# Kernel optimization log

Hardware: AMD Instinct MI355X
Metric: run time of the kernel (lower is better)

Reference implementation:

```python
import jax, jax.numpy as jnp
import numpy as np
from jax import lax

T, B, C, H, W = 8, 32, 256, 32, 32
EPS = 1e-12


def setup_inputs() -> dict:
    key = jax.random.key(0)
    k1, k2, k3, k4 = jax.random.split(key, 4)
    return {
        "x_accum": jax.random.normal(k1, (T, B, C, H, W), dtype=jnp.float32),
        "prev_scale": jax.random.uniform(k2, (C,), dtype=jnp.float32, minval=0.1, maxval=1.0),
        "prev_bias": jax.random.normal(k3, (C,), dtype=jnp.float32),
        "vth": jax.random.uniform(k4, (C,), dtype=jnp.float32, minval=0.5, maxval=1.5),
        "tau": jnp.ones((1,), dtype=jnp.float32) * 4.0,
        "is_first_layer": 0,
    }


def reference(x_accum, prev_scale, prev_bias, vth, tau, is_first_layer):
    # per-channel views broadcasting over [B, C, H, W]
    s = prev_scale.reshape(1, C, 1, 1)
    b = prev_bias.reshape(1, C, 1, 1)
    v = vth.reshape(1, C, 1, 1)
    tau = tau.reshape(())  # scalar
    bias_scaled = jnp.round(b * tau / (s + EPS))
    vth_scaled = jnp.round(v * tau / (s + EPS))

    drive = x_accum if is_first_layer else x_accum * tau  # [T, B, C, H, W]

    def step(mem, x_t):
        mem = mem + x_t + bias_scaled
        spike = (mem >= vth_scaled).astype(x_accum.dtype)
        mem = mem - spike * vth_scaled  # soft reset
        return mem, spike

    mem0 = jnp.zeros_like(x_accum[0])
    _, spikes = lax.scan(step, mem0, drive)
    return spikes  # [T, B, C, H, W]
```

## Files before the change

kernel.cpp:

```cpp
#include <hip/hip_runtime.h>


#define T_STEPS 8
#define C_CH    256
#define HW      1024
#define EPS_F   1e-12f

typedef float v4f __attribute__((ext_vector_type(4)));

__global__ __launch_bounds__(256) void integer_neuron_kernel(
    const float* __restrict__ x,
    const float* __restrict__ prev_scale,
    const float* __restrict__ prev_bias,
    const float* __restrict__ vth,
    const float* __restrict__ tau_p,
    const int*   __restrict__ is_first_p,
    float* __restrict__ out,
    long long n_planes)
{
    const float tau      = tau_p[0];
    const int   is_first = is_first_p[0];
    const float drive_mul = is_first ? 1.0f : tau;

    const long long plane = (long long)blockIdx.x;
    const int c = (int)(plane % C_CH);

    const float denom       = __fadd_rn(prev_scale[c], EPS_F);
    const float bias_scaled = rintf(__fdiv_rn(__fmul_rn(prev_bias[c], tau), denom));
    const float vth_scaled  = rintf(__fdiv_rn(__fmul_rn(vth[c],       tau), denom));

    const long long N    = n_planes * (long long)HW;
    const long long base = plane * (long long)HW + (long long)threadIdx.x * 4;

    float mx = 0.0f, my = 0.0f, mz = 0.0f, mw = 0.0f;

    #pragma unroll
    for (int t = 0; t < T_STEPS; ++t) {
        const long long off = (long long)t * N + base;
        const v4f xv = __builtin_nontemporal_load(
            reinterpret_cast<const v4f*>(x + off));

        v4f sp;

        mx    = __fadd_rn(__fadd_rn(mx, __fmul_rn(xv.x, drive_mul)), bias_scaled);
        sp.x  = (mx >= vth_scaled) ? 1.0f : 0.0f;
        mx    = __fsub_rn(mx, __fmul_rn(sp.x, vth_scaled));
        my    = __fadd_rn(__fadd_rn(my, __fmul_rn(xv.y, drive_mul)), bias_scaled);
        sp.y  = (my >= vth_scaled) ? 1.0f : 0.0f;
        my    = __fsub_rn(my, __fmul_rn(sp.y, vth_scaled));
        mz    = __fadd_rn(__fadd_rn(mz, __fmul_rn(xv.z, drive_mul)), bias_scaled);
        sp.z  = (mz >= vth_scaled) ? 1.0f : 0.0f;
        mz    = __fsub_rn(mz, __fmul_rn(sp.z, vth_scaled));
        mw    = __fadd_rn(__fadd_rn(mw, __fmul_rn(xv.w, drive_mul)), bias_scaled);
        sp.w  = (mw >= vth_scaled) ? 1.0f : 0.0f;
        mw    = __fsub_rn(mw, __fmul_rn(sp.w, vth_scaled));

        __builtin_nontemporal_store(sp, reinterpret_cast<v4f*>(out + off));
    }
}

extern "C" void kernel_launch(void* const* d_in, const int* in_sizes, int n_in,
                              void* d_out, int out_size, void* d_ws, size_t ws_size,
                              hipStream_t stream) {
    const float* x          = (const float*)d_in[0];
    const float* prev_scale = (const float*)d_in[1];
    const float* prev_bias  = (const float*)d_in[2];
    const float* vth        = (const float*)d_in[3];
    const float* tau        = (const float*)d_in[4];
    const int*   is_first   = (const int*)d_in[5];
    float* out = (float*)d_out;

    const long long total    = (long long)out_size;
    const long long n_planes = total / ((long long)T_STEPS * HW);

    dim3 grid((unsigned)n_planes);
    dim3 block(256);
    integer_neuron_kernel<<<grid, block, 0, stream>>>(
        x, prev_scale, prev_bias, vth, tau, is_first, out, n_planes);
}
```

Before: 100.1 us.

## Map one wavefront per plane with four vec4 loads per thread per step

Each 256-thread block now covers four channel planes, one 64-lane wavefront per plane. Each thread handles four float4 positions strided by 256 floats, so it issues four independent 16-byte loads per timestep. The grid shrinks by four. The aim is more memory-level parallelism per thread and fewer blocks for this bandwidth-bound kernel, at the cost of more registers and fewer resident waves.

```diff
diff --git a/kernel.cpp b/kernel.cpp
--- a/kernel.cpp
+++ b/kernel.cpp
@@ -5,6 +5,7 @@
 #define C_CH    256
 #define HW      1024
 #define EPS_F   1e-12f
+#define NPOS    4
 
 typedef float v4f __attribute__((ext_vector_type(4)));
 
@@ -22,7 +23,7 @@
     const int   is_first = is_first_p[0];
     const float drive_mul = is_first ? 1.0f : tau;
 
-    const long long plane = (long long)blockIdx.x;
+    const long long plane = (long long)blockIdx.x * 4 + (threadIdx.x >> 6);
     const int c = (int)(plane % C_CH);
 
     const float denom       = __fadd_rn(prev_scale[c], EPS_F);
@@ -30,32 +31,43 @@
     const float vth_scaled  = rintf(__fdiv_rn(__fmul_rn(vth[c],       tau), denom));
 
     const long long N    = n_planes * (long long)HW;
-    const long long base = plane * (long long)HW + (long long)threadIdx.x * 4;
+    const long long base = plane * (long long)HW
+                         + (long long)(threadIdx.x & 63) * 4;
 
-    float mx = 0.0f, my = 0.0f, mz = 0.0f, mw = 0.0f;
+    float mem[NPOS][4];
+    #pragma unroll
+    for (int p = 0; p < NPOS; ++p)
+        #pragma unroll
+        for (int j = 0; j < 4; ++j)
+            mem[p][j] = 0.0f;
 
     #pragma unroll
     for (int t = 0; t < T_STEPS; ++t) {
         const long long off = (long long)t * N + base;
-        const v4f xv = __builtin_nontemporal_load(
-            reinterpret_cast<const v4f*>(x + off));
 
-        v4f sp;
+        v4f xv[NPOS];
+        #pragma unroll
+        for (int p = 0; p < NPOS; ++p)
+            xv[p] = __builtin_nontemporal_load(
+                reinterpret_cast<const v4f*>(x + off + p * 256));
 
-        mx    = __fadd_rn(__fadd_rn(mx, __fmul_rn(xv.x, drive_mul)), bias_scaled);
-        sp.x  = (mx >= vth_scaled) ? 1.0f : 0.0f;
-        mx    = __fsub_rn(mx, __fmul_rn(sp.x, vth_scaled));
-        my    = __fadd_rn(__fadd_rn(my, __fmul_rn(xv.y, drive_mul)), bias_scaled);
-        sp.y  = (my >= vth_scaled) ? 1.0f : 0.0f;
-        my    = __fsub_rn(my, __fmul_rn(sp.y, vth_scaled));
-        mz    = __fadd_rn(__fadd_rn(mz, __fmul_rn(xv.z, drive_mul)), bias_scaled);
-        sp.z  = (mz >= vth_scaled) ? 1.0f : 0.0f;
-        mz    = __fsub_rn(mz, __fmul_rn(sp.z, vth_scaled));
-        mw    = __fadd_rn(__fadd_rn(mw, __fmul_rn(xv.w, drive_mul)), bias_scaled);
-        sp.w  = (mw >= vth_scaled) ? 1.0f : 0.0f;
-        mw    = __fsub_rn(mw, __fmul_rn(sp.w, vth_scaled));
+        v4f sp[NPOS];
+        #pragma unroll
+        for (int p = 0; p < NPOS; ++p) {
+            #pragma unroll
+            for (int j = 0; j < 4; ++j) {
+                float m = mem[p][j];
+                m = __fadd_rn(__fadd_rn(m, __fmul_rn(xv[p][j], drive_mul)), bias_scaled);
+                const float s = (m >= vth_scaled) ? 1.0f : 0.0f;
+                mem[p][j] = __fsub_rn(m, __fmul_rn(s, vth_scaled));
+                sp[p][j] = s;
+            }
+        }
 
-        __builtin_nontemporal_store(sp, reinterpret_cast<v4f*>(out + off));
+        #pragma unroll
+        for (int p = 0; p < NPOS; ++p)
+            __builtin_nontemporal_store(sp[p],
+                reinterpret_cast<v4f*>(out + off + p * 256));
     }
 }
 
@@ -73,7 +85,7 @@
     const long long total    = (long long)out_size;
     const long long n_planes = total / ((long long)T_STEPS * HW);
 
-    dim3 grid((unsigned)n_planes);
+    dim3 grid((unsigned)(n_planes / 4));
     dim3 block(256);
     integer_neuron_kernel<<<grid, block, 0, stream>>>(
         x, prev_scale, prev_bias, vth, tau, is_first, out, n_planes);
```

After: 89.63 us, median of 2. -10.5%, faster.
